# Kernel optimization log

Hardware: AMD Instinct MI355X
Metric: run time of the kernel (lower is better)

The kernel has to match this reference:

```python
import jax, jax.numpy as jnp
import numpy as np

NUM_GENO = 16384
NUM_ENV = 53
R = 2666
B = 256
EPS = 1e-5


def setup_inputs() -> dict:
    key = jax.random.key(0)
    ks = jax.random.split(key, 12)

    def w(k, shape, fan_in):
        return jax.random.normal(k, shape, dtype=jnp.float32) / np.float32(np.sqrt(fan_in))

    f32 = jnp.float32
    return {
        "x": jax.random.normal(ks[0], (B, NUM_GENO + NUM_ENV), dtype=f32),
        "W1": w(ks[1], (R, NUM_GENO), NUM_GENO), "b1": jnp.zeros((R,), f32),
        "Wmid": w(ks[2], (11, R, R), R), "bmid": jnp.zeros((11, R), f32),
        "bn_g": jnp.ones((12, R), f32), "bn_b": jnp.zeros((12, R), f32),
        "bn_rm": jnp.zeros((12, R), f32), "bn_rv": jnp.ones((12, R), f32),
        "Wlin": w(ks[3], (R, 54, NUM_ENV + 1), NUM_ENV + 1), "blin": jnp.zeros((R, 54), f32),
        "W13": w(ks[4], (54, 54), 54), "b13": jnp.zeros((54,), f32),
        "W14": w(ks[5], (54, 54), 54), "b14": jnp.zeros((54,), f32),
        "W15": w(ks[6], (5, 54), 54), "b15": jnp.zeros((5,), f32),
        "bn3_g": jnp.ones((3, R), f32), "bn3_b": jnp.zeros((3, R), f32),
        "bn3_rm": jnp.zeros((3, R), f32), "bn3_rv": jnp.ones((3, R), f32),
        "W16": w(ks[7], (750, R * 5), R * 5), "b16": jnp.zeros((750,), f32),
        "W17": w(ks[8], (750, 750), 750), "b17": jnp.zeros((750,), f32),
        "W18": w(ks[9], (750, 750), 750), "b18": jnp.zeros((750,), f32),
    }


def reference(x, W1, b1, Wmid, bmid, bn_g, bn_b, bn_rm, bn_rv, Wlin, blin,
              W13, b13, W14, b14, W15, b15, bn3_g, bn3_b, bn3_rm, bn3_rv,
              W16, b16, W17, b17, W18, b18):
    relu = jax.nn.relu

    def bn(h, i):  # BatchNorm1d eval over [B, R]
        return (h - bn_rm[i]) * jax.lax.rsqrt(bn_rv[i] + EPS) * bn_g[i] + bn_b[i]

    env = x[:, NUM_GENO:]           # [B, NUM_ENV]
    h = x[:, :NUM_GENO]             # [B, NUM_GENO]

    h = relu(bn(h @ W1.T + b1, 0))  # fc1; dropout = identity (eval)
    d = h
    k = 0
    for _block in range(5):         # residual blocks: (fc2,fc3) ... (fc10,fc11)
        for _ in range(2):
            h = relu(bn(h @ Wmid[k].T + bmid[k], k + 1))
            k += 1
        h = d + h
        d = h
    h = relu(bn(h @ Wmid[10].T + bmid[10], 11))  # fc12

    # 2666 per-feature tiny Linears fused into one batched GEMM
    # z[b,i,:] = concat(env[b], h[b,i])  -> [B, R, NUM_ENV+1]
    z = jnp.concatenate(
        [jnp.broadcast_to(env[:, None, :], (B, R, NUM_ENV)), h[:, :, None]], axis=-1)
    d3 = jnp.einsum('bif,iof->bio', z, Wlin) + blin[None]  # [B, R, 54]

    def bn3(h3, j):  # BatchNorm1d eval over [B, R, C]: channels = dim 1 (R)
        return ((h3 - bn3_rm[j][None, :, None])
                * jax.lax.rsqrt(bn3_rv[j][None, :, None] + EPS)
                * bn3_g[j][None, :, None] + bn3_b[j][None, :, None])

    h3 = relu(bn3(d3 @ W13.T + b13, 0))
    h3 = relu(bn3(h3 @ W14.T + b14, 1))
    h3 = relu(bn3(h3 @ W15.T + b15, 2))   # [B, R, 5]

    h = h3.reshape(B, -1)                  # [B, R*5]
    h = relu(h @ W16.T + b16)
    h = relu(h @ W17.T + b17)
    h = relu(h @ W18.T + b18)
    return h
```

## Files before the change

### kernel.cpp

```cpp
#include <hip/hip_runtime.h>

#define EPS 1e-5f

typedef __attribute__((ext_vector_type(8))) short s8v;
typedef __attribute__((ext_vector_type(4))) float f4v;

__device__ __forceinline__ unsigned short f2b(float x) {
  unsigned int u = __float_as_uint(x);
  u += 0x7FFFu + ((u >> 16) & 1u);
  return (unsigned short)(u >> 16);
}
__device__ __forceinline__ float b2f(unsigned short b) {
  return __uint_as_float(((unsigned int)b) << 16);
}

__global__ __launch_bounds__(256)
void gemm_splitk(const unsigned short* __restrict__ A, int lda,
                 const float* __restrict__ B, int ldb,
                 float* __restrict__ P, int NT, int N, int K, int kchunk, int KS)
{
  __shared__ unsigned short As[256 * 40];
  __shared__ unsigned short Bs[64 * 40];
  const int bid = (int)blockIdx.x;
  const int ky = bid % KS, ntp = bid / KS;
  const int n0 = ntp << 6;
  const int t = threadIdx.x, lane = t & 63, w = t >> 6;
  const int lr = lane & 15, lk = lane >> 4;

  const int kstart = ky * kchunk;
  const int kend = min(K, kstart + kchunk);
  const int nfull = (kend - kstart) >> 5;
  const int rem = (kend - kstart) & 31;

  const int ar0 = t >> 2, akc = t & 3;
  const int br0 = t >> 2, bq = t & 3;

  f4v acc[4][4] = {};
  s8v a_cur[4]; float2 b_cur[4];
  s8v a_nxt[4]; float2 b_nxt[4];

  auto loadA = [&](s8v* dst, int kb) {
    #pragma unroll
    for (int j = 0; j < 4; ++j)
      dst[j] = *(const s8v*)(A + (size_t)(ar0 + j * 64) * lda + kb + akc * 8);
  };
  auto loadB = [&](float2* dst, int kb) {
    const int row = n0 + br0;
    const int kk = kb + bq * 8;
    if (row < N) {
      #pragma unroll
      for (int j = 0; j < 4; ++j)
        dst[j] = *(const float2*)(B + (size_t)row * ldb + kk + 2 * j);
    } else {
      #pragma unroll
      for (int j = 0; j < 4; ++j) { dst[j].x = 0.f; dst[j].y = 0.f; }
    }
  };
  auto stage = [&](const s8v* av, const float2* bv) {
    #pragma unroll
    for (int j = 0; j < 4; ++j)
      *(s8v*)(As + (ar0 + j * 64) * 40 + akc * 8) = av[j];
    s8v pk;
    #pragma unroll
    for (int j = 0; j < 4; ++j) {
      pk[2 * j]     = (short)f2b(bv[j].x);
      pk[2 * j + 1] = (short)f2b(bv[j].y);
    }
    *(s8v*)(Bs + br0 * 40 + bq * 8) = pk;
  };
  auto domfma = [&]() {
    s8v af[4];
    #pragma unroll
    for (int fm = 0; fm < 4; ++fm)
      af[fm] = *(const s8v*)(As + (w * 64 + fm * 16 + lr) * 40 + lk * 8);
    #pragma unroll
    for (int fn = 0; fn < 4; ++fn) {
      s8v bf = *(const s8v*)(Bs + (fn * 16 + lr) * 40 + lk * 8);
      #pragma unroll
      for (int fm = 0; fm < 4; ++fm)
        acc[fm][fn] = __builtin_amdgcn_mfma_f32_16x16x32_bf16(af[fm], bf, acc[fm][fn], 0, 0, 0);
    }
  };

  int kb = kstart;
  if (nfull > 0) {
    loadA(a_cur, kb); loadB(b_cur, kb);
    for (int s = 0; s < nfull; ++s) {
      stage(a_cur, b_cur);
      __syncthreads();
      const bool more = (s + 1 < nfull);
      if (more) { loadA(a_nxt, kb + 32); loadB(b_nxt, kb + 32); }
      domfma();
      __syncthreads();
      if (more) {
        #pragma unroll
        for (int j = 0; j < 4; ++j) a_cur[j] = a_nxt[j];
        #pragma unroll
        for (int j = 0; j < 4; ++j) b_cur[j] = b_nxt[j];
        kb += 32;
      }
    }
    kb += 32;
  }
  if (rem) {
    loadA(a_cur, kb);
    {
      const int row = n0 + br0;
      const int kk = kb + bq * 8;
      #pragma unroll
      for (int j = 0; j < 4; ++j) {
        const int k0 = kk + 2 * j;
        b_cur[j].x = (row < N && k0     < kend) ? B[(size_t)row * ldb + k0]     : 0.f;
        b_cur[j].y = (row < N && k0 + 1 < kend) ? B[(size_t)row * ldb + k0 + 1] : 0.f;
      }
    }
    stage(a_cur, b_cur);
    __syncthreads();
    domfma();
    __syncthreads();
  }

  #pragma unroll
  for (int fn = 0; fn < 4; ++fn) {
    float* Pk = P + ((size_t)ky * NT + (ntp * 2 + (fn >> 1))) * 8192;
    const int lcol = (fn & 1) * 16 + lr;
    #pragma unroll
    for (int fm = 0; fm < 4; ++fm)
      #pragma unroll
      for (int j = 0; j < 4; ++j) {
        const int row = w * 64 + fm * 16 + lk * 4 + j;
        Pk[row * 32 + lcol] = acc[fm][fn][j];
      }
  }
}

template<bool BN, bool RES, bool WRD, bool WRT, bool F32OUT>
__global__ __launch_bounds__(256)
void reduce_k(const float* __restrict__ P, int KS, int NT, int N,
              const float* __restrict__ bias,
              const float* __restrict__ g, const float* __restrict__ bb,
              const float* __restrict__ rm, const float* __restrict__ rv,
              float* __restrict__ dR, int lddr,
              unsigned short* __restrict__ Cb, int ldc,
              unsigned short* __restrict__ Ct, float* __restrict__ Cf)
{
  const int bid = (int)blockIdx.x;
  const int nt = bid >> 2, rpart = bid & 3;
  const int n0 = nt << 5;
  const int t = threadIdx.x;
  const float* Pt = P + (size_t)nt * 8192;

  #pragma unroll
  for (int q = 0; q < 2; ++q) {
    const int i4 = rpart * 512 + q * 256 + t;
    const int row = i4 >> 3;
    const int cb = (i4 & 7) * 4;
    float vv[4] = {0.f, 0.f, 0.f, 0.f};
    for (int kk = 0; kk < KS; ++kk) {
      const float4 pv = *(const float4*)(Pt + (size_t)kk * NT * 8192 + (size_t)i4 * 4);
      vv[0] += pv.x; vv[1] += pv.y; vv[2] += pv.z; vv[3] += pv.w;
    }
    #pragma unroll
    for (int e = 0; e < 4; ++e) {
      const int col = n0 + cb + e;
      if (col >= N) {
        if (!WRT && !F32OUT) Cb[(size_t)row * ldc + col] = 0;
        continue;
      }
      float v = vv[e] + bias[col];
      if (BN) { const float s = g[col] * rsqrtf(rv[col] + EPS); v = (v - rm[col]) * s + bb[col]; }
      v = fmaxf(v, 0.f);
      if (RES) v += dR[(size_t)row * lddr + col];
      if (WRD) dR[(size_t)row * lddr + col] = v;
      if (F32OUT) Cf[(size_t)row * N + col] = v;
      else if (WRT) Ct[(size_t)col * 256 + row] = f2b(v);
      else Cb[(size_t)row * ldc + col] = f2b(v);
    }
  }
}

__global__ __launch_bounds__(256)
void prep_k(const float* __restrict__ x, unsigned short* __restrict__ xg,
            unsigned short* __restrict__ envb, unsigned short* __restrict__ h5b)
{
  const int bid = (int)blockIdx.x, t = threadIdx.x;
  if (bid < 16384) {
    const int idx = bid * 256 + t;
    const int r = idx >> 14, c = idx & 16383;
    xg[idx] = f2b(x[(size_t)r * 16437 + c]);
  } else if (bid < 16456) {
    const int idx = (bid - 16384) * 256 + t;
    const int b = idx / 72, c = idx % 72;
    envb[idx] = (c < 53) ? f2b(x[(size_t)b * 16437 + 16384 + c]) : (unsigned short)0;
  } else {
    for (int z = t; z < 256 * 14; z += 256) {
      const int b = z / 14, j = z % 14;
      h5b[(size_t)b * 13344 + 13330 + j] = 0;
    }
  }
}

__global__ __launch_bounds__(256, 2)
void fused_head(const unsigned short* __restrict__ envb,
                const unsigned short* __restrict__ htr,
                const float* __restrict__ Wlin, const float* __restrict__ blin,
                const float* __restrict__ W13, const float* __restrict__ b13,
                const float* __restrict__ W14, const float* __restrict__ b14,
                const float* __restrict__ W15, const float* __restrict__ b15,
                const float* __restrict__ bn3g, const float* __restrict__ bn3b,
                const float* __restrict__ bn3rm, const float* __restrict__ bn3rv,
                unsigned short* __restrict__ h5b)
{
  __shared__ unsigned short act[256 * 72];
  __shared__ unsigned short Wl[64 * 72];
  __shared__ unsigned short Wa[64 * 72];
  __shared__ unsigned short Wb[16 * 72];
  const int i = (int)blockIdx.x;
  const int t = threadIdx.x, lane = t & 63, w = t >> 6;
  const int lr = lane & 15, lk = lane >> 4;
  const int R = 2666;

  #pragma unroll
  for (int c8 = 0; c8 < 9; ++c8)
    *(s8v*)(act + t * 72 + c8 * 8) = *(const s8v*)(envb + t * 72 + c8 * 8);
  act[t * 72 + 53] = htr[(size_t)i * 256 + t];

  const float* wli = Wlin + (size_t)i * 2916;
  for (int idx = t; idx < 64 * 72; idx += 256) {
    const int r = idx / 72, f = idx % 72;
    Wl[idx] = (r < 54 && f < 54) ? f2b(wli[r * 54 + f]) : (unsigned short)0;
    Wa[idx] = (r < 54 && f < 54) ? f2b(W13[r * 54 + f]) : (unsigned short)0;
  }
  for (int idx = t; idx < 16 * 72; idx += 256) {
    const int r = idx / 72, f = idx % 72;
    Wb[idx] = (r < 5 && f < 54) ? f2b(W15[r * 54 + f]) : (unsigned short)0;
  }
  const float s0 = bn3g[i] * rsqrtf(bn3rv[i] + EPS), m0 = bn3rm[i], c0 = bn3b[i];
  const float s1 = bn3g[R+i] * rsqrtf(bn3rv[R+i] + EPS), m1 = bn3rm[R+i], c1 = bn3b[R+i];
  const float s2 = bn3g[2*R+i] * rsqrtf(bn3rv[2*R+i] + EPS), m2 = bn3rm[2*R+i], c2 = bn3b[2*R+i];
  __syncthreads();

  const int abase = (w * 64 + lr) * 72 + lk * 8;
  f4v acc[4][4];

  auto zacc = [&]() {
    #pragma unroll
    for (int a = 0; a < 4; ++a)
      #pragma unroll
      for (int b = 0; b < 4; ++b) acc[a][b] = f4v{0.f, 0.f, 0.f, 0.f};
  };
  auto gemm4 = [&](const unsigned short* B) {
    s8v af[2][4];
    #pragma unroll
    for (int ks = 0; ks < 2; ++ks)
      #pragma unroll
      for (int fm = 0; fm < 4; ++fm)
        af[ks][fm] = *(const s8v*)(act + abase + fm * 16 * 72 + ks * 32);
    #pragma unroll
    for (int fn = 0; fn < 4; ++fn) {
      s8v b0 = *(const s8v*)(B + (fn * 16 + lr) * 72 + lk * 8);
      s8v b1 = *(const s8v*)(B + (fn * 16 + lr) * 72 + 32 + lk * 8);
      #pragma unroll
      for (int fm = 0; fm < 4; ++fm) {
        acc[fm][fn] = __builtin_amdgcn_mfma_f32_16x16x32_bf16(af[0][fm], b0, acc[fm][fn], 0, 0, 0);
        acc[fm][fn] = __builtin_amdgcn_mfma_f32_16x16x32_bf16(af[1][fm], b1, acc[fm][fn], 0, 0, 0);
      }
    }
  };
  auto epi_bn = [&](const float* bias, float s, float m, float c) {
    #pragma unroll
    for (int fn = 0; fn < 4; ++fn) {
      const int o = fn * 16 + lr;
      const float bo = (o < 54) ? bias[o] : 0.f;
      #pragma unroll
      for (int fm = 0; fm < 4; ++fm)
        #pragma unroll
        for (int j = 0; j < 4; ++j) {
          const int row = w * 64 + fm * 16 + lk * 4 + j;
          float v = acc[fm][fn][j] + bo;
          v = (v - m) * s + c;
          v = fmaxf(v, 0.f);
          act[row * 72 + o] = (o < 54) ? f2b(v) : (unsigned short)0;
        }
    }
  };

  zacc(); gemm4(Wl);
  #pragma unroll
  for (int fn = 0; fn < 4; ++fn) {
    const int o = fn * 16 + lr;
    const float bl = (o < 54) ? blin[(size_t)i * 54 + o] : 0.f;
    #pragma unroll
    for (int fm = 0; fm < 4; ++fm)
      #pragma unroll
      for (int j = 0; j < 4; ++j) {
        const int row = w * 64 + fm * 16 + lk * 4 + j;
        float v = acc[fm][fn][j] + bl;
        act[row * 72 + o] = (o < 54) ? f2b(v) : (unsigned short)0;
      }
  }
  __syncthreads();
  for (int idx = t; idx < 64 * 72; idx += 256) {
    const int r = idx / 72, f = idx % 72;
    Wl[idx] = (r < 54 && f < 54) ? f2b(W14[r * 54 + f]) : (unsigned short)0;
  }
  zacc(); gemm4(Wa); epi_bn(b13, s0, m0, c0);
  __syncthreads();
  zacc(); gemm4(Wl); epi_bn(b14, s1, m1, c1);
  f4v a4[4] = {};
  {
    s8v af[2][4];
    #pragma unroll
    for (int ks = 0; ks < 2; ++ks)
      #pragma unroll
      for (int fm = 0; fm < 4; ++fm)
        af[ks][fm] = *(const s8v*)(act + abase + fm * 16 * 72 + ks * 32);
    s8v b0 = *(const s8v*)(Wb + lr * 72 + lk * 8);
    s8v b1 = *(const s8v*)(Wb + lr * 72 + 32 + lk * 8);
    #pragma unroll
    for (int fm = 0; fm < 4; ++fm) {
      a4[fm] = __builtin_amdgcn_mfma_f32_16x16x32_bf16(af[0][fm], b0, a4[fm], 0, 0, 0);
      a4[fm] = __builtin_amdgcn_mfma_f32_16x16x32_bf16(af[1][fm], b1, a4[fm], 0, 0, 0);
    }
  }
  if (lr < 5) {
    const float b5 = b15[lr];
    #pragma unroll
    for (int fm = 0; fm < 4; ++fm)
      #pragma unroll
      for (int j = 0; j < 4; ++j) {
        const int row = w * 64 + fm * 16 + lk * 4 + j;
        float v = a4[fm][j] + b5;
        v = (v - m2) * s2 + c2;
        v = fmaxf(v, 0.f);
        h5b[(size_t)row * 13344 + (size_t)i * 5 + lr] = f2b(v);
      }
  }
}

extern "C" void kernel_launch(void* const* d_in, const int* in_sizes, int n_in,
                              void* d_out, int out_size, void* d_ws, size_t ws_size,
                              hipStream_t stream)
{
  const float* x    = (const float*)d_in[0];
  const float* W1   = (const float*)d_in[1];
  const float* b1   = (const float*)d_in[2];
  const float* Wmid = (const float*)d_in[3];
  const float* bmid = (const float*)d_in[4];
  const float* bng  = (const float*)d_in[5];
  const float* bnb  = (const float*)d_in[6];
  const float* bnrm = (const float*)d_in[7];
  const float* bnrv = (const float*)d_in[8];
  const float* Wlin = (const float*)d_in[9];
  const float* blin = (const float*)d_in[10];
  const float* W13  = (const float*)d_in[11];
  const float* b13  = (const float*)d_in[12];
  const float* W14  = (const float*)d_in[13];
  const float* b14  = (const float*)d_in[14];
  const float* W15  = (const float*)d_in[15];
  const float* b15  = (const float*)d_in[16];
  const float* bn3g = (const float*)d_in[17];
  const float* bn3b = (const float*)d_in[18];
  const float* bn3rm= (const float*)d_in[19];
  const float* bn3rv= (const float*)d_in[20];
  const float* W16  = (const float*)d_in[21];
  const float* b16  = (const float*)d_in[22];
  const float* W17  = (const float*)d_in[23];
  const float* b17  = (const float*)d_in[24];
  const float* W18  = (const float*)d_in[25];
  const float* b18  = (const float*)d_in[26];

  const int R = 2666;
  char* p = (char*)d_ws;
  unsigned short* xg  = (unsigned short*)p; p += (size_t)256 * 16384 * 2;
  unsigned short* hA  = (unsigned short*)p; p += (size_t)256 * 2688 * 2;
  unsigned short* hB  = (unsigned short*)p; p += (size_t)256 * 2688 * 2;
  float*          dR  = (float*)p;          p += (size_t)256 * 2688 * 4;
  unsigned short* h5b = (unsigned short*)p; p += (size_t)256 * 13344 * 2;
  unsigned short* h6b = (unsigned short*)p; p += (size_t)256 * 768 * 2;
  unsigned short* h7b = (unsigned short*)p; p += (size_t)256 * 768 * 2;
  unsigned short* envb= (unsigned short*)p; p += (size_t)256 * 72 * 2;
  unsigned short* htr = (unsigned short*)p; p += (size_t)2666 * 256 * 2;
  float* P = (float*)p;

  dim3 TB(256);

  prep_k<<<dim3(16457), TB, 0, stream>>>(x, xg, envb, h5b);

  gemm_splitk<<<dim3(42 * 8), TB, 0, stream>>>(xg, 16384, W1, 16384, P, 84, R, 16384, 2048, 8);
  reduce_k<true, false, true, false, false><<<dim3(84 * 4), TB, 0, stream>>>(
      P, 8, 84, R, b1, bng, bnb, bnrm, bnrv, dR, 2688, hA, 2688, nullptr, nullptr);

  unsigned short* cur = hA; unsigned short* nxt = hB;
  for (int k = 0; k < 11; ++k) {
    const float* bw = Wmid + (size_t)k * R * R;
    const float* bs = bmid + (size_t)k * R;
    const int L = k + 1;
    gemm_splitk<<<dim3(42 * 10), TB, 0, stream>>>(cur, 2688, bw, R, P, 84, R, R, 288, 10);
    if (k == 10)
      reduce_k<true, false, false, true, false><<<dim3(84 * 4), TB, 0, stream>>>(
          P, 10, 84, R, bs, bng + (size_t)L * R, bnb + (size_t)L * R,
          bnrm + (size_t)L * R, bnrv + (size_t)L * R,
          nullptr, 0, nullptr, 2688, htr, nullptr);
    else if ((k & 1) == 0)
      reduce_k<true, false, false, false, false><<<dim3(84 * 4), TB, 0, stream>>>(
          P, 10, 84, R, bs, bng + (size_t)L * R, bnb + (size_t)L * R,
          bnrm + (size_t)L * R, bnrv + (size_t)L * R,
          nullptr, 0, nxt, 2688, nullptr, nullptr);
    else
      reduce_k<true, true, true, false, false><<<dim3(84 * 4), TB, 0, stream>>>(
          P, 10, 84, R, bs, bng + (size_t)L * R, bnb + (size_t)L * R,
          bnrm + (size_t)L * R, bnrv + (size_t)L * R,
          dR, 2688, nxt, 2688, nullptr, nullptr);
    unsigned short* tmp = cur; cur = nxt; nxt = tmp;
  }

  fused_head<<<dim3(2666), TB, 0, stream>>>(
      envb, htr, Wlin, blin, W13, b13, W14, b14, W15, b15,
      bn3g, bn3b, bn3rm, bn3rv, h5b);

  gemm_splitk<<<dim3(12 * 27), TB, 0, stream>>>(h5b, 13344, W16, 13330, P, 24, 750, 13330, 512, 27);
  reduce_k<false, false, false, false, false><<<dim3(24 * 4), TB, 0, stream>>>(
      P, 27, 24, 750, b16, nullptr, nullptr, nullptr, nullptr,
      nullptr, 0, h6b, 768, nullptr, nullptr);

  gemm_splitk<<<dim3(12 * 8), TB, 0, stream>>>(h6b, 768, W17, 750, P, 24, 750, 750, 96, 8);
  reduce_k<false, false, false, false, false><<<dim3(24 * 4), TB, 0, stream>>>(
      P, 8, 24, 750, b17, nullptr, nullptr, nullptr, nullptr,
      nullptr, 0, h7b, 768, nullptr, nullptr);

  gemm_splitk<<<dim3(12 * 8), TB, 0, stream>>>(h7b, 768, W18, 750, P, 24, 750, 750, 96, 8);
  reduce_k<false, false, false, false, true><<<dim3(24 * 4), TB, 0, stream>>>(
      P, 8, 24, 750, b18, nullptr, nullptr, nullptr, nullptr,
      nullptr, 0, nullptr, 768, nullptr, (float*)d_out);
}
```

Measured before the change: 644.0 us.

## Use BK=64 split-K GEMM with bf16 partials and vectorized reduce

```diff
diff --git a/kernel.cpp b/kernel.cpp
--- a/kernel.cpp
+++ b/kernel.cpp
@@ -15,12 +15,13 @@
 }
 
 __global__ __launch_bounds__(256)
-void gemm_splitk(const unsigned short* __restrict__ A, int lda,
-                 const float* __restrict__ B, int ldb,
-                 float* __restrict__ P, int NT, int N, int K, int kchunk, int KS)
+void gemm_bk64(const unsigned short* __restrict__ A, int lda,
+               const float* __restrict__ B, int ldb,
+               unsigned short* __restrict__ Pb,
+               int NPAIR, int N, int K, int kchunk, int KS)
 {
-  __shared__ unsigned short As[256 * 40];
-  __shared__ unsigned short Bs[64 * 40];
+  __shared__ unsigned short As[256 * 72];
+  __shared__ unsigned short Bs[64 * 72];
   const int bid = (int)blockIdx.x;
   const int ky = bid % KS, ntp = bid / KS;
   const int n0 = ntp << 6;
@@ -29,153 +30,176 @@
 
   const int kstart = ky * kchunk;
   const int kend = min(K, kstart + kchunk);
-  const int nfull = (kend - kstart) >> 5;
-  const int rem = (kend - kstart) & 31;
-
-  const int ar0 = t >> 2, akc = t & 3;
-  const int br0 = t >> 2, bq = t & 3;
+  const int len = kend - kstart;
+  const int nfull = len >> 6;
+  const int rem = len & 63;
+
+  const int ar = t >> 2, ac = t & 3;
+  const int br = t >> 2, bq = t & 3;
 
   f4v acc[4][4] = {};
-  s8v a_cur[4]; float2 b_cur[4];
-  s8v a_nxt[4]; float2 b_nxt[4];
-
-  auto loadA = [&](s8v* dst, int kb) {
-    #pragma unroll
-    for (int j = 0; j < 4; ++j)
-      dst[j] = *(const s8v*)(A + (size_t)(ar0 + j * 64) * lda + kb + akc * 8);
-  };
-  auto loadB = [&](float2* dst, int kb) {
-    const int row = n0 + br0;
-    const int kk = kb + bq * 8;
+  float4 b_cur[4], b_nxt[4];
+
+  auto loadB = [&](float4* dst, int kb) {
+    const int row = n0 + br;
     if (row < N) {
       #pragma unroll
-      for (int j = 0; j < 4; ++j)
-        dst[j] = *(const float2*)(B + (size_t)row * ldb + kk + 2 * j);
+      for (int i = 0; i < 4; ++i)
+        dst[i] = *(const float4*)(B + (size_t)row * ldb + kb + bq * 16 + i * 4);
     } else {
       #pragma unroll
-      for (int j = 0; j < 4; ++j) { dst[j].x = 0.f; dst[j].y = 0.f; }
-    }
-  };
-  auto stage = [&](const s8v* av, const float2* bv) {
-    #pragma unroll
-    for (int j = 0; j < 4; ++j)
-      *(s8v*)(As + (ar0 + j * 64) * 40 + akc * 8) = av[j];
-    s8v pk;
-    #pragma unroll
-    for (int j = 0; j < 4; ++j) {
-      pk[2 * j]     = (short)f2b(bv[j].x);
-      pk[2 * j + 1] = (short)f2b(bv[j].y);
-    }
-    *(s8v*)(Bs + br0 * 40 + bq * 8) = pk;
+      for (int i = 0; i < 4; ++i) { dst[i].x = dst[i].y = dst[i].z = dst[i].w = 0.f; }
+    }
+  };
+  auto stageA = [&](int kb) {
+    #pragma unroll
+    for (int p = 0; p < 4; ++p) {
+      const int row = ar + p * 64;
+      const s8v v0 = *(const s8v*)(A + (size_t)row * lda + kb + ac * 16);
+      const s8v v1 = *(const s8v*)(A + (size_t)row * lda + kb + ac * 16 + 8);
+      *(s8v*)(As + row * 72 + ac * 16) = v0;
+      *(s8v*)(As + row * 72 + ac * 16 + 8) = v1;
+    }
+  };
+  auto stageB = [&](const float4* bv) {
+    s8v p0, p1;
+    #pragma unroll
+    for (int i = 0; i < 4; ++i) {
+      p0[i]     = (short)f2b(bv[i >> 1].x);
+    }
+    p0[0] = (short)f2b(bv[0].x); p0[1] = (short)f2b(bv[0].y);
+    p0[2] = (short)f2b(bv[0].z); p0[3] = (short)f2b(bv[0].w);
+    p0[4] = (short)f2b(bv[1].x); p0[5] = (short)f2b(bv[1].y);
+    p0[6] = (short)f2b(bv[1].z); p0[7] = (short)f2b(bv[1].w);
+    p1[0] = (short)f2b(bv[2].x); p1[1] = (short)f2b(bv[2].y);
+    p1[2] = (short)f2b(bv[2].z); p1[3] = (short)f2b(bv[2].w);
+    p1[4] = (short)f2b(bv[3].x); p1[5] = (short)f2b(bv[3].y);
+    p1[6] = (short)f2b(bv[3].z); p1[7] = (short)f2b(bv[3].w);
+    *(s8v*)(Bs + br * 72 + bq * 16) = p0;
+    *(s8v*)(Bs + br * 72 + bq * 16 + 8) = p1;
   };
   auto domfma = [&]() {
-    s8v af[4];
-    #pragma unroll
-    for (int fm = 0; fm < 4; ++fm)
-      af[fm] = *(const s8v*)(As + (w * 64 + fm * 16 + lr) * 40 + lk * 8);
-    #pragma unroll
-    for (int fn = 0; fn < 4; ++fn) {
-      s8v bf = *(const s8v*)(Bs + (fn * 16 + lr) * 40 + lk * 8);
+    #pragma unroll
+    for (int ks = 0; ks < 2; ++ks) {
+      s8v af[4], bf[4];
       #pragma unroll
       for (int fm = 0; fm < 4; ++fm)
-        acc[fm][fn] = __builtin_amdgcn_mfma_f32_16x16x32_bf16(af[fm], bf, acc[fm][fn], 0, 0, 0);
+        af[fm] = *(const s8v*)(As + (w * 64 + fm * 16 + lr) * 72 + ks * 32 + lk * 8);
+      #pragma unroll
+      for (int fn = 0; fn < 4; ++fn)
+        bf[fn] = *(const s8v*)(Bs + (fn * 16 + lr) * 72 + ks * 32 + lk * 8);
+      #pragma unroll
+      for (int fm = 0; fm < 4; ++fm)
+        #pragma unroll
+        for (int fn = 0; fn < 4; ++fn)
+          acc[fm][fn] = __builtin_amdgcn_mfma_f32_16x16x32_bf16(af[fm], bf[fn], acc[fm][fn], 0, 0, 0);
     }
   };
 
   int kb = kstart;
   if (nfull > 0) {
-    loadA(a_cur, kb); loadB(b_cur, kb);
+    loadB(b_cur, kb);
     for (int s = 0; s < nfull; ++s) {
-      stage(a_cur, b_cur);
+      stageA(kb);
+      stageB(b_cur);
       __syncthreads();
       const bool more = (s + 1 < nfull);
-      if (more) { loadA(a_nxt, kb + 32); loadB(b_nxt, kb + 32); }
+      if (more) loadB(b_nxt, kb + 64);
       domfma();
       __syncthreads();
       if (more) {
         #pragma unroll
-        for (int j = 0; j < 4; ++j) a_cur[j] = a_nxt[j];
+        for (int i = 0; i < 4; ++i) b_cur[i] = b_nxt[i];
+        kb += 64;
+      }
+    }
+    kb += 64;
+  }
+  if (rem) {
+    stageA(kb);
+    {
+      const int row = n0 + br;
+      #pragma unroll
+      for (int i = 0; i < 4; ++i) {
+        float e[4];
         #pragma unroll
-        for (int j = 0; j < 4; ++j) b_cur[j] = b_nxt[j];
-        kb += 32;
-      }
-    }
-    kb += 32;
-  }
-  if (rem) {
-    loadA(a_cur, kb);
-    {
-      const int row = n0 + br0;
-      const int kk = kb + bq * 8;
-      #pragma unroll
-      for (int j = 0; j < 4; ++j) {
-        const int k0 = kk + 2 * j;
-        b_cur[j].x = (row < N && k0     < kend) ? B[(size_t)row * ldb + k0]     : 0.f;
-        b_cur[j].y = (row < N && k0 + 1 < kend) ? B[(size_t)row * ldb + k0 + 1] : 0.f;
-      }
-    }
-    stage(a_cur, b_cur);
+        for (int v = 0; v < 4; ++v) {
+          const int c = kb + bq * 16 + i * 4 + v;
+          e[v] = (row < N && c < kend) ? B[(size_t)row * ldb + c] : 0.f;
+        }
+        b_cur[i].x = e[0]; b_cur[i].y = e[1]; b_cur[i].z = e[2]; b_cur[i].w = e[3];
+      }
+    }
+    stageB(b_cur);
     __syncthreads();
     domfma();
     __syncthreads();
   }
 
+  unsigned short* Pt = Pb + ((size_t)ky * NPAIR + ntp) * 16384;
   #pragma unroll
-  for (int fn = 0; fn < 4; ++fn) {
-    float* Pk = P + ((size_t)ky * NT + (ntp * 2 + (fn >> 1))) * 8192;
-    const int lcol = (fn & 1) * 16 + lr;
-    #pragma unroll
-    for (int fm = 0; fm < 4; ++fm)
+  for (int fm = 0; fm < 4; ++fm)
+    #pragma unroll
+    for (int fn = 0; fn < 4; ++fn) {
+      const int col = fn * 16 + lr;
       #pragma unroll
       for (int j = 0; j < 4; ++j) {
         const int row = w * 64 + fm * 16 + lk * 4 + j;
-        Pk[row * 32 + lcol] = acc[fm][fn][j];
-      }
-  }
+        Pt[row * 64 + col] = f2b(acc[fm][fn][j]);
+      }
+    }
 }
 
 template<bool BN, bool RES, bool WRD, bool WRT, bool F32OUT>
 __global__ __launch_bounds__(256)
-void reduce_k(const float* __restrict__ P, int KS, int NT, int N,
-              const float* __restrict__ bias,
-              const float* __restrict__ g, const float* __restrict__ bb,
-              const float* __restrict__ rm, const float* __restrict__ rv,
-              float* __restrict__ dR, int lddr,
-              unsigned short* __restrict__ Cb, int ldc,
-              unsigned short* __restrict__ Ct, float* __restrict__ Cf)
+void reduce_bk64(const unsigned short* __restrict__ Pb, int KS, int NPAIR, int N,
+                 const float* __restrict__ bias,
+                 const float* __restrict__ g, const float* __restrict__ bb,
+                 const float* __restrict__ rm, const float* __restrict__ rv,
+                 float* __restrict__ dR, int lddr,
+                 unsigned short* __restrict__ Cb, int ldc,
+                 unsigned short* __restrict__ Ct, float* __restrict__ Cf)
 {
   const int bid = (int)blockIdx.x;
-  const int nt = bid >> 2, rpart = bid & 3;
-  const int n0 = nt << 5;
+  const int ntp = bid >> 2, qr = bid & 3;
   const int t = threadIdx.x;
-  const float* Pt = P + (size_t)nt * 8192;
-
+  const int row = qr * 64 + (t >> 2);
+  const int c0 = (t & 3) * 16;
+  const int n0 = ntp << 6;
+
+  float vv[16];
   #pragma unroll
-  for (int q = 0; q < 2; ++q) {
-    const int i4 = rpart * 512 + q * 256 + t;
-    const int row = i4 >> 3;
-    const int cb = (i4 & 7) * 4;
-    float vv[4] = {0.f, 0.f, 0.f, 0.f};
-    for (int kk = 0; kk < KS; ++kk) {
-      const float4 pv = *(const float4*)(Pt + (size_t)kk * NT * 8192 + (size_t)i4 * 4);
-      vv[0] += pv.x; vv[1] += pv.y; vv[2] += pv.z; vv[3] += pv.w;
-    }
-    #pragma unroll
-    for (int e = 0; e < 4; ++e) {
-      const int col = n0 + cb + e;
-      if (col >= N) {
-        if (!WRT && !F32OUT) Cb[(size_t)row * ldc + col] = 0;
-        continue;
-      }
-      float v = vv[e] + bias[col];
+  for (int e = 0; e < 16; ++e) vv[e] = 0.f;
+
+  const unsigned short* base = Pb + (size_t)ntp * 16384 + row * 64 + c0;
+  for (int ky = 0; ky < KS; ++ky) {
+    const s8v pa = *(const s8v*)(base + (size_t)ky * NPAIR * 16384);
+    const s8v pb2 = *(const s8v*)(base + (size_t)ky * NPAIR * 16384 + 8);
+    #pragma unroll
+    for (int e = 0; e < 8; ++e) vv[e]     += b2f((unsigned short)pa[e]);
+    #pragma unroll
+    for (int e = 0; e < 8; ++e) vv[8 + e] += b2f((unsigned short)pb2[e]);
+  }
+
+  unsigned short outp[16];
+  #pragma unroll
+  for (int e = 0; e < 16; ++e) {
+    const int col = n0 + c0 + e;
+    float v = 0.f;
+    if (col < N) {
+      v = vv[e] + bias[col];
       if (BN) { const float s = g[col] * rsqrtf(rv[col] + EPS); v = (v - rm[col]) * s + bb[col]; }
       v = fmaxf(v, 0.f);
       if (RES) v += dR[(size_t)row * lddr + col];
       if (WRD) dR[(size_t)row * lddr + col] = v;
       if (F32OUT) Cf[(size_t)row * N + col] = v;
       else if (WRT) Ct[(size_t)col * 256 + row] = f2b(v);
-      else Cb[(size_t)row * ldc + col] = f2b(v);
-    }
+    }
+    outp[e] = f2b(v);
+  }
+  if (!F32OUT && !WRT) {
+    *(s8v*)(Cb + (size_t)row * ldc + n0 + c0) = *(const s8v*)(outp);
+    *(s8v*)(Cb + (size_t)row * ldc + n0 + c0 + 8) = *(const s8v*)(outp + 8);
   }
 }
 
@@ -193,9 +217,9 @@
     const int b = idx / 72, c = idx % 72;
     envb[idx] = (c < 53) ? f2b(x[(size_t)b * 16437 + 16384 + c]) : (unsigned short)0;
   } else {
-    for (int z = t; z < 256 * 14; z += 256) {
-      const int b = z / 14, j = z % 14;
-      h5b[(size_t)b * 13344 + 13330 + j] = 0;
+    for (int z = t; z < 256 * 46; z += 256) {
+      const int b = z / 46, j = z % 46;
+      h5b[(size_t)b * 13376 + 13330 + j] = 0;
     }
   }
 }
@@ -333,7 +357,7 @@
         float v = a4[fm][j] + b5;
         v = (v - m2) * s2 + c2;
         v = fmaxf(v, 0.f);
-        h5b[(size_t)row * 13344 + (size_t)i * 5 + lr] = f2b(v);
+        h5b[(size_t)row * 13376 + (size_t)i * 5 + lr] = f2b(v);
       }
   }
 }
@@ -376,40 +400,40 @@
   unsigned short* hA  = (unsigned short*)p; p += (size_t)256 * 2688 * 2;
   unsigned short* hB  = (unsigned short*)p; p += (size_t)256 * 2688 * 2;
   float*          dR  = (float*)p;          p += (size_t)256 * 2688 * 4;
-  unsigned short* h5b = (unsigned short*)p; p += (size_t)256 * 13344 * 2;
+  unsigned short* h5b = (unsigned short*)p; p += (size_t)256 * 13376 * 2;
   unsigned short* h6b = (unsigned short*)p; p += (size_t)256 * 768 * 2;
   unsigned short* h7b = (unsigned short*)p; p += (size_t)256 * 768 * 2;
   unsigned short* envb= (unsigned short*)p; p += (size_t)256 * 72 * 2;
   unsigned short* htr = (unsigned short*)p; p += (size_t)2666 * 256 * 2;
-  float* P = (float*)p;
+  unsigned short* Pb  = (unsigned short*)p;
 
   dim3 TB(256);
 
   prep_k<<<dim3(16457), TB, 0, stream>>>(x, xg, envb, h5b);
 
-  gemm_splitk<<<dim3(42 * 8), TB, 0, stream>>>(xg, 16384, W1, 16384, P, 84, R, 16384, 2048, 8);
-  reduce_k<true, false, true, false, false><<<dim3(84 * 4), TB, 0, stream>>>(
-      P, 8, 84, R, b1, bng, bnb, bnrm, bnrv, dR, 2688, hA, 2688, nullptr, nullptr);
+  gemm_bk64<<<dim3(42 * 8), TB, 0, stream>>>(xg, 16384, W1, 16384, Pb, 42, R, 16384, 2048, 8);
+  reduce_bk64<true, false, true, false, false><<<dim3(42 * 4), TB, 0, stream>>>(
+      Pb, 8, 42, R, b1, bng, bnb, bnrm, bnrv, dR, 2688, hA, 2688, nullptr, nullptr);
 
   unsigned short* cur = hA; unsigned short* nxt = hB;
   for (int k = 0; k < 11; ++k) {
     const float* bw = Wmid + (size_t)k * R * R;
     const float* bs = bmid + (size_t)k * R;
     const int L = k + 1;
-    gemm_splitk<<<dim3(42 * 10), TB, 0, stream>>>(cur, 2688, bw, R, P, 84, R, R, 288, 10);
+    gemm_bk64<<<dim3(42 * 14), TB, 0, stream>>>(cur, 2688, bw, R, Pb, 42, R, R, 192, 14);
     if (k == 10)
-      reduce_k<true, false, false, true, false><<<dim3(84 * 4), TB, 0, stream>>>(
-          P, 10, 84, R, bs, bng + (size_t)L * R, bnb + (size_t)L * R,
+      reduce_bk64<true, false, false, true, false><<<dim3(42 * 4), TB, 0, stream>>>(
+          Pb, 14, 42, R, bs, bng + (size_t)L * R, bnb + (size_t)L * R,
           bnrm + (size_t)L * R, bnrv + (size_t)L * R,
           nullptr, 0, nullptr, 2688, htr, nullptr);
     else if ((k & 1) == 0)
-      reduce_k<true, false, false, false, false><<<dim3(84 * 4), TB, 0, stream>>>(
-          P, 10, 84, R, bs, bng + (size_t)L * R, bnb + (size_t)L * R,
+      reduce_bk64<true, false, false, false, false><<<dim3(42 * 4), TB, 0, stream>>>(
+          Pb, 14, 42, R, bs, bng + (size_t)L * R, bnb + (size_t)L * R,
           bnrm + (size_t)L * R, bnrv + (size_t)L * R,
           nullptr, 0, nxt, 2688, nullptr, nullptr);
     else
-      reduce_k<true, true, true, false, false><<<dim3(84 * 4), TB, 0, stream>>>(
-          P, 10, 84, R, bs, bng + (size_t)L * R, bnb + (size_t)L * R,
+      reduce_bk64<true, true, true, false, false><<<dim3(42 * 4), TB, 0, stream>>>(
+          Pb, 14, 42, R, bs, bng + (size_t)L * R, bnb + (size_t)L * R,
           bnrm + (size_t)L * R, bnrv + (size_t)L * R,
           dR, 2688, nxt, 2688, nullptr, nullptr);
     unsigned short* tmp = cur; cur = nxt; nxt = tmp;
@@ -419,18 +443,18 @@
       envb, htr, Wlin, blin, W13, b13, W14, b14, W15, b15,
       bn3g, bn3b, bn3rm, bn3rv, h5b);
 
-  gemm_splitk<<<dim3(12 * 27), TB, 0, stream>>>(h5b, 13344, W16, 13330, P, 24, 750, 13330, 512, 27);
-  reduce_k<false, false, false, false, false><<<dim3(24 * 4), TB, 0, stream>>>(
-      P, 27, 24, 750, b16, nullptr, nullptr, nullptr, nullptr,
+  gemm_bk64<<<dim3(12 * 15), TB, 0, stream>>>(h5b, 13376, W16, 13330, Pb, 12, 750, 13330, 896, 15);
+  reduce_bk64<false, false, false, false, false><<<dim3(12 * 4), TB, 0, stream>>>(
+      Pb, 15, 12, 750, b16, nullptr, nullptr, nullptr, nullptr,
       nullptr, 0, h6b, 768, nullptr, nullptr);
 
-  gemm_splitk<<<dim3(12 * 8), TB, 0, stream>>>(h6b, 768, W17, 750, P, 24, 750, 750, 96, 8);
-  reduce_k<false, false, false, false, false><<<dim3(24 * 4), TB, 0, stream>>>(
-      P, 8, 24, 750, b17, nullptr, nullptr, nullptr, nullptr,
+  gemm_bk64<<<dim3(12 * 6), TB, 0, stream>>>(h6b, 768, W17, 750, Pb, 12, 750, 750, 128, 6);
+  reduce_bk64<false, false, false, false, false><<<dim3(12 * 4), TB, 0, stream>>>(
+      Pb, 6, 12, 750, b17, nullptr, nullptr, nullptr, nullptr,
       nullptr, 0, h7b, 768, nullptr, nullptr);
 
-  gemm_splitk<<<dim3(12 * 8), TB, 0, stream>>>(h7b, 768, W18, 750, P, 24, 750, 750, 96, 8);
-  reduce_k<false, false, false, false, true><<<dim3(24 * 4), TB, 0, stream>>>(
-      P, 8, 24, 750, b18, nullptr, nullptr, nullptr, nullptr,
+  gemm_bk64<<<dim3(12 * 6), TB, 0, stream>>>(h7b, 768, W18, 750, Pb, 12, 750, 750, 128, 6);
+  reduce_bk64<false, false, false, false, true><<<dim3(12 * 4), TB, 0, stream>>>(
+      Pb, 6, 12, 750, b18, nullptr, nullptr, nullptr, nullptr,
       nullptr, 0, nullptr, 768, nullptr, (float*)d_out);
 }
```

After: 605.0 us. 6.0% less time.
